# Kernel optimization log

Measured on AMD Instinct MI355X. Metric: run time of the kernel, lower is better.

Reference implementation:

```python
import jax, jax.numpy as jnp
import numpy as np
import math

B, T, C, H = 4, 1024, 1024, 16
D = C // H
EPS = 1e-5


def layer_norm(x, w, b):
    mu = jnp.mean(x, axis=-1, keepdims=True)
    var = jnp.mean(jnp.square(x - mu), axis=-1, keepdims=True)
    return (x - mu) * jax.lax.rsqrt(var + EPS) * w + b


def setup_inputs() -> dict:
    key = jax.random.key(0)
    ks = jax.random.split(key, 8)
    s = 0.02
    return {
        "x": jax.random.normal(ks[0], (B, T, C), jnp.float32),
        "attention_mask": jnp.ones((B, T), jnp.float32),
        "ln1_w": jnp.ones((C,), jnp.float32),
        "ln1_b": jnp.zeros((C,), jnp.float32),
        "w_attn": jax.random.normal(ks[1], (C, 3 * C), jnp.float32) * s,
        "b_attn": jnp.zeros((3 * C,), jnp.float32),
        "w_proj": jax.random.normal(ks[2], (C, C), jnp.float32) * s,
        "b_proj": jnp.zeros((C,), jnp.float32),
        "threshold": jnp.float32(0.0005),  # (layer_idx+1)/n_layer * final_token_threshold
        "ln2_w": jnp.ones((C,), jnp.float32),
        "ln2_b": jnp.zeros((C,), jnp.float32),
        "w_fc": jax.random.normal(ks[3], (C, 4 * C), jnp.float32) * s,
        "b_fc": jnp.zeros((4 * C,), jnp.float32),
        "w_fc2": jax.random.normal(ks[4], (4 * C, C), jnp.float32) * s,
        "b_fc2": jnp.zeros((C,), jnp.float32),
    }


def reference(x, attention_mask, ln1_w, ln1_b, w_attn, b_attn, w_proj, b_proj,
              threshold, ln2_w, ln2_b, w_fc, b_fc, w_fc2, b_fc2):
    # ---- attention (eval mode, dropout=0; hard masking_mode) ----
    h = layer_norm(x, ln1_w, ln1_b)
    qkv = h @ w_attn + b_attn                      # (B,T,3C)
    q, k, v = jnp.split(qkv, 3, axis=-1)
    q = q.reshape(B, T, H, D).transpose(0, 2, 1, 3)  # (B,H,T,D)
    k = k.reshape(B, T, H, D).transpose(0, 2, 1, 3)
    v = v.reshape(B, T, H, D).transpose(0, 2, 1, 3)

    scale = 1.0 / math.sqrt(D)
    logits = jnp.einsum("bhqd,bhkd->bhqk", q, k) * scale  # (B,H,T,T)
    causal = jnp.tril(jnp.ones((T, T), bool))
    neg_inf = jnp.float32(-jnp.inf)
    logits = jnp.where(causal[None, None], logits, neg_inf)
    # key-side validity mask (applied in original's manual pass; mask is all-ones
    # here so flash-path y == softmax(causal logits) @ v as well)
    logits = jnp.where(attention_mask[:, None, None, :] == 0, neg_inf, logits)
    att = jax.nn.softmax(logits, axis=-1)

    y = jnp.einsum("bhqk,bhkd->bhqd", att, v)      # (B,H,T,D)
    importance = att.mean(axis=1).mean(axis=1)     # (B,T): mean over heads, then queries

    y = y.transpose(0, 2, 1, 3).reshape(B, T, C)
    x = x + (y @ w_proj + b_proj)

    # ---- hard pruning mask ----
    pruning_mask = (importance >= threshold).astype(x.dtype)
    combined_mask = attention_mask * pruning_mask
    x = x * combined_mask[:, :, None]

    # ---- MLP ----
    h2 = layer_norm(x, ln2_w, ln2_b)
    f = jax.nn.gelu(h2 @ w_fc + b_fc, approximate=False)
    x = x + (f @ w_fc2 + b_fc2)

    pruning_loss = jnp.float32(0.0)  # hard mode -> always 0
    return (x, combined_mask, pruning_loss)
```

## Files before the change

### kernel.cpp

```cpp
#include <hip/hip_runtime.h>
#include <cstdint>
#include <cstring>

typedef unsigned short u16;
typedef short bf16x8 __attribute__((ext_vector_type(8)));
typedef float f32x4 __attribute__((ext_vector_type(4)));

#define MFMA16(a,b,c) __builtin_amdgcn_mfma_f32_16x16x32_bf16(a,b,c,0,0,0)


__device__ __forceinline__ u16 f2bf(float f) {
  union { float f; uint32_t u; } un; un.f = f;
  uint32_t u = un.u;
  u += 0x7FFFu + ((u >> 16) & 1u);
  return (u16)(u >> 16);
}

__device__ __forceinline__ void gl_lds16(const void* g, void* l) {
  __builtin_amdgcn_global_load_lds(
      (__attribute__((address_space(1))) void*)(const_cast<void*>(g)),
      (__attribute__((address_space(3))) void*)l, 16, 0, 0);
}


__global__ __launch_bounds__(256) void transpose_to_bf16(
    const float* __restrict__ W, u16* __restrict__ Wt, int K, int N)
{
  __shared__ float tile[32][33];
  int kt = blockIdx.y * 32, nt = blockIdx.x * 32;
  int tx = threadIdx.x, ty = threadIdx.y;
#pragma unroll
  for (int i = 0; i < 4; ++i)
    tile[ty + i * 8][tx] = W[(size_t)(kt + ty + i * 8) * N + nt + tx];
  __syncthreads();
#pragma unroll
  for (int i = 0; i < 4; ++i)
    Wt[(size_t)(nt + ty + i * 8) * K + kt + tx] = f2bf(tile[tx][ty + i * 8]);
}


__global__ __launch_bounds__(256) void ln_bf16(
    const float* __restrict__ x, const float* __restrict__ wt,
    const float* __restrict__ bs, u16* __restrict__ out)
{
  int row = blockIdx.x;
  int tid = threadIdx.x, lane = tid & 63, w = tid >> 6;
  const float* xr = x + (size_t)row * 1024;
  float4 v = *(const float4*)(xr + tid * 4);
  float s = v.x + v.y + v.z + v.w;
  float sq = v.x * v.x + v.y * v.y + v.z * v.z + v.w * v.w;
#pragma unroll
  for (int o = 1; o < 64; o <<= 1) { s += __shfl_xor(s, o); sq += __shfl_xor(sq, o); }
  __shared__ float ls[4], lq[4];
  if (lane == 0) { ls[w] = s; lq[w] = sq; }
  __syncthreads();
  s = ls[0] + ls[1] + ls[2] + ls[3];
  sq = lq[0] + lq[1] + lq[2] + lq[3];
  float mu = s * (1.f / 1024.f);
  float var = sq * (1.f / 1024.f) - mu * mu;
  float rstd = rsqrtf(var + 1e-5f);
  float4 wv = *(const float4*)(wt + tid * 4);
  float4 bv = *(const float4*)(bs + tid * 4);
  ushort4 o4;
  o4.x = f2bf((v.x - mu) * rstd * wv.x + bv.x);
  o4.y = f2bf((v.y - mu) * rstd * wv.y + bv.y);
  o4.z = f2bf((v.z - mu) * rstd * wv.z + bv.z);
  o4.w = f2bf((v.w - mu) * rstd * wv.w + bv.w);
  *(ushort4*)(out + (size_t)row * 1024 + tid * 4) = o4;
}


__device__ __forceinline__ void gemm_mainloop_db(
    const u16* __restrict__ Abase, const u16* __restrict__ Bbase,
    int lda, int ldb, int nIter, f32x4 acc[4][4])
{
  __shared__ __align__(16) u16 lA[2][128 * 32];
  __shared__ __align__(16) u16 lB[2][128 * 32];

  const int tid = threadIdx.x;
  const int lane = tid & 63;
  const int w = tid >> 6;
  const int wr = (w >> 1) * 64;
  const int wc = (w & 1) * 64;
  const int laneM = lane & 15;
  const int laneK = (lane >> 4) * 8;

#pragma unroll
  for (int i = 0; i < 4; ++i)
#pragma unroll
    for (int j = 0; j < 4; ++j)
      acc[i][j] = f32x4{0.f, 0.f, 0.f, 0.f};

  const int off0 = w * 1024 + lane * 16;
  const int off1 = off0 + 4096;
  const int rA0 = off0 >> 6, cb0 = off0 & 63;
  const int rA1 = off1 >> 6, cb1 = off1 & 63;

  const size_t sA = (size_t)lda * 2;
  const size_t sB = (size_t)ldb * 2;
  const char* pA0 = (const char*)Abase + (size_t)rA0 * sA + cb0;
  const char* pA1 = (const char*)Abase + (size_t)rA1 * sA + cb1;
  const char* pB0 = (const char*)Bbase + (size_t)rA0 * sB + cb0;
  const char* pB1 = (const char*)Bbase + (size_t)rA1 * sB + cb1;
  char* dA0 = (char*)&lA[0][0] + off0;
  char* dA1 = (char*)&lA[0][0] + off1;
  char* dB0 = (char*)&lB[0][0] + off0;
  char* dB1 = (char*)&lB[0][0] + off1;

  gl_lds16(pA0, dA0); gl_lds16(pA1, dA1);
  gl_lds16(pB0, dB0); gl_lds16(pB1, dB1);
  pA0 += 64; pA1 += 64; pB0 += 64; pB1 += 64;
  __syncthreads();

  for (int it = 0; it < nIter; ++it) {
    const int cur = it & 1;
    const int nb = cur ^ 1;
    if (it + 1 < nIter) {
      gl_lds16(pA0, dA0 + nb * 8192);
      gl_lds16(pA1, dA1 + nb * 8192);
      gl_lds16(pB0, dB0 + nb * 8192);
      gl_lds16(pB1, dB1 + nb * 8192);
      pA0 += 64; pA1 += 64; pB0 += 64; pB1 += 64;
    }
    const u16* aRd = &lA[cur][(wr + laneM) * 32 + laneK];
    const u16* bRd = &lB[cur][(wc + laneM) * 32 + laneK];
    bf16x8 af[4], bfr[4];
#pragma unroll
    for (int t = 0; t < 4; ++t) {
      af[t]  = *(const bf16x8*)(aRd + t * 16 * 32);
      bfr[t] = *(const bf16x8*)(bRd + t * 16 * 32);
    }
#pragma unroll
    for (int i = 0; i < 4; ++i)
#pragma unroll
      for (int j = 0; j < 4; ++j)
        acc[i][j] = MFMA16(af[i], bfr[j], acc[i][j]);
    if (it + 1 < nIter) __syncthreads();
  }
}


__global__ __launch_bounds__(256) void gemm_qkv(
    const u16* __restrict__ A, const u16* __restrict__ Bt,
    const float* __restrict__ bias,
    u16* __restrict__ qo, u16* __restrict__ ko, u16* __restrict__ vo)
{
  f32x4 acc[4][4];
  int m0 = blockIdx.y * 128, n0 = blockIdx.x * 128;
  gemm_mainloop_db(A + (size_t)m0 * 1024, Bt + (size_t)n0 * 1024, 1024, 1024, 32, acc);
  const int lane = threadIdx.x & 63, w = threadIdx.x >> 6;
  const int wr = (w >> 1) * 64, wc = (w & 1) * 64;
  const int laneM = lane & 15, q4 = lane >> 4;
  const int which = (n0 >> 10);
#pragma unroll
  for (int ti = 0; ti < 4; ++ti) {
#pragma unroll
    for (int tj = 0; tj < 4; ++tj) {
      int n = n0 + wc + tj * 16 + laneM;
      int c = n & 1023;
      int hh = c >> 6, d = c & 63;
      float bval = bias[n];
      if (which == 2) {
        int m0r = m0 + wr + ti * 16 + q4 * 4;
        int b = m0r >> 10, t0 = m0r & 1023;
        ushort4 o4;
        o4.x = f2bf(acc[ti][tj][0] + bval);
        o4.y = f2bf(acc[ti][tj][1] + bval);
        o4.z = f2bf(acc[ti][tj][2] + bval);
        o4.w = f2bf(acc[ti][tj][3] + bval);
        *(ushort4*)&vo[((size_t)((b * 16 + hh) * 64 + d)) * 1024 + t0] = o4;
      } else {
        u16* dst = (which == 0) ? qo : ko;
#pragma unroll
        for (int r = 0; r < 4; ++r) {
          int m = m0 + wr + ti * 16 + q4 * 4 + r;
          int b = m >> 10, t = m & 1023;
          dst[((size_t)((b * 16 + hh) * 1024 + t)) * 64 + d] = f2bf(acc[ti][tj][r] + bval);
        }
      }
    }
  }
}

__global__ __launch_bounds__(256) void gemm_proj(
    const u16* __restrict__ A, const u16* __restrict__ Bt,
    const float* __restrict__ bias, const float* __restrict__ xin,
    const float* __restrict__ maskv, float* __restrict__ x2)
{
  f32x4 acc[4][4];
  int m0 = blockIdx.y * 128, n0 = blockIdx.x * 128;
  gemm_mainloop_db(A + (size_t)m0 * 1024, Bt + (size_t)n0 * 1024, 1024, 1024, 32, acc);
  const int lane = threadIdx.x & 63, w = threadIdx.x >> 6;
  const int wr = (w >> 1) * 64, wc = (w & 1) * 64;
  const int laneM = lane & 15, q4 = lane >> 4;
#pragma unroll
  for (int ti = 0; ti < 4; ++ti) {
#pragma unroll
    for (int tj = 0; tj < 4; ++tj) {
      int n = n0 + wc + tj * 16 + laneM;
      float bval = bias[n];
#pragma unroll
      for (int r = 0; r < 4; ++r) {
        int m = m0 + wr + ti * 16 + q4 * 4 + r;
        float v = xin[(size_t)m * 1024 + n] + acc[ti][tj][r] + bval;
        x2[(size_t)m * 1024 + n] = v * maskv[m];
      }
    }
  }
}

__global__ __launch_bounds__(256) void gemm_fc(
    const u16* __restrict__ A, const u16* __restrict__ Bt,
    const float* __restrict__ bias, u16* __restrict__ fo)
{
  f32x4 acc[4][4];
  int m0 = blockIdx.y * 128, n0 = blockIdx.x * 128;
  gemm_mainloop_db(A + (size_t)m0 * 1024, Bt + (size_t)n0 * 1024, 1024, 1024, 32, acc);
  const int lane = threadIdx.x & 63, w = threadIdx.x >> 6;
  const int wr = (w >> 1) * 64, wc = (w & 1) * 64;
  const int laneM = lane & 15, q4 = lane >> 4;
#pragma unroll
  for (int ti = 0; ti < 4; ++ti) {
#pragma unroll
    for (int tj = 0; tj < 4; ++tj) {
      int n = n0 + wc + tj * 16 + laneM;
      float bval = bias[n];
#pragma unroll
      for (int r = 0; r < 4; ++r) {
        int m = m0 + wr + ti * 16 + q4 * 4 + r;
        float v = acc[ti][tj][r] + bval;
        float g = 0.5f * v * (1.f + erff(v * 0.70710678118654752f));
        fo[(size_t)m * 4096 + n] = f2bf(g);
      }
    }
  }
}

__global__ __launch_bounds__(256) void prefill_out(
    const float* __restrict__ x2, const float* __restrict__ bias,
    float* __restrict__ out)
{
  int i = blockIdx.x * 256 + threadIdx.x;
  int col4 = i & 255;
  float4 v = ((const float4*)x2)[i];
  float4 b = ((const float4*)bias)[col4];
  float4 o; o.x = v.x + b.x; o.y = v.y + b.y; o.z = v.z + b.z; o.w = v.w + b.w;
  ((float4*)out)[i] = o;
}

__global__ __launch_bounds__(256) void gemm_fc2_splitk(
    const u16* __restrict__ A, const u16* __restrict__ Bt,
    float* __restrict__ out)
{
  f32x4 acc[4][4];
  int m0 = blockIdx.y * 128, n0 = blockIdx.x * 128, k0 = blockIdx.z * 1024;
  gemm_mainloop_db(A + (size_t)m0 * 4096 + k0, Bt + (size_t)n0 * 4096 + k0,
                   4096, 4096, 32, acc);
  const int lane = threadIdx.x & 63, w = threadIdx.x >> 6;
  const int wr = (w >> 1) * 64, wc = (w & 1) * 64;
  const int laneM = lane & 15, q4 = lane >> 4;
#pragma unroll
  for (int ti = 0; ti < 4; ++ti) {
#pragma unroll
    for (int tj = 0; tj < 4; ++tj) {
      int n = n0 + wc + tj * 16 + laneM;
#pragma unroll
      for (int r = 0; r < 4; ++r) {
        int m = m0 + wr + ti * 16 + q4 * 4 + r;
        atomicAdd(&out[(size_t)m * 1024 + n], acc[ti][tj][r]);
      }
    }
  }
}


__global__ __launch_bounds__(256) void attn_fwd(
    const u16* __restrict__ qb, const u16* __restrict__ kb, const u16* __restrict__ vtb,
    u16* __restrict__ yb, float* __restrict__ part)
{
  const int bh = blockIdx.x;
  const int qbi = 15 - blockIdx.y;
  const int b = bh >> 4, h = bh & 15;
  const int tid = threadIdx.x, lane = tid & 63, w = tid >> 6;
  const int q0 = qbi * 64;
  const int laneM = lane & 15, q4 = lane >> 4;
  const float scale = 0.125f;

  __shared__ __align__(16) u16 lK[64 * 72];
  __shared__ __align__(16) u16 lV[64 * 72];
  __shared__ __align__(16) u16 lP[4][16 * 72];

  const u16* qrow = qb + ((size_t)(bh * 1024 + q0 + w * 16 + laneM)) * 64 + q4 * 8;
  bf16x8 qf0 = *(const bf16x8*)qrow;
  bf16x8 qf1 = *(const bf16x8*)(qrow + 32);

  const int nkt = qbi + 1;
  const int srow = tid >> 3;
  const int scol = (tid & 7) * 8;
  const u16* kbase = kb + (size_t)bh * 65536;
  const u16* vbase = vtb + (size_t)bh * 65536;

  float lrow[4] = {0.f, 0.f, 0.f, 0.f};
  for (int kt = 0; kt < nkt; ++kt) {
#pragma unroll
    for (int p = 0; p < 2; ++p) {
      int row = srow + p * 32;
      *(uint4*)&lK[row * 72 + scol] =
          *(const uint4*)(kbase + (size_t)(kt * 64 + row) * 64 + scol);
    }
    __syncthreads();
#pragma unroll
    for (int tj = 0; tj < 4; ++tj) {
      const u16* kp = &lK[(tj * 16 + laneM) * 72 + q4 * 8];
      bf16x8 k0 = *(const bf16x8*)kp;
      bf16x8 k1 = *(const bf16x8*)(kp + 32);
      f32x4 z = {0.f, 0.f, 0.f, 0.f};
      z = MFMA16(qf0, k0, z);
      z = MFMA16(qf1, k1, z);
      int kc = kt * 64 + tj * 16 + laneM;
#pragma unroll
      for (int r = 0; r < 4; ++r) {
        int qg = q0 + w * 16 + q4 * 4 + r;
        lrow[r] += (kc <= qg) ? __expf(z[r] * scale) : 0.f;
      }
    }
    __syncthreads();
  }
  float linv[4];
#pragma unroll
  for (int r = 0; r < 4; ++r) {
    float s = lrow[r];
    s += __shfl_xor(s, 1); s += __shfl_xor(s, 2);
    s += __shfl_xor(s, 4); s += __shfl_xor(s, 8);
    linv[r] = 1.f / s;
  }

  f32x4 o_[4];
#pragma unroll
  for (int dt = 0; dt < 4; ++dt) o_[dt] = f32x4{0.f, 0.f, 0.f, 0.f};

  for (int kt = 0; kt < nkt; ++kt) {
#pragma unroll
    for (int p = 0; p < 2; ++p) {
      int row = srow + p * 32;
      *(uint4*)&lK[row * 72 + scol] =
          *(const uint4*)(kbase + (size_t)(kt * 64 + row) * 64 + scol);
      *(uint4*)&lV[row * 72 + scol] =
          *(const uint4*)(vbase + (size_t)row * 1024 + kt * 64 + scol);
    }
    __syncthreads();
    u16* lPw = &lP[w][0];
#pragma unroll
    for (int tj = 0; tj < 4; ++tj) {
      const u16* kp = &lK[(tj * 16 + laneM) * 72 + q4 * 8];
      bf16x8 k0 = *(const bf16x8*)kp;
      bf16x8 k1 = *(const bf16x8*)(kp + 32);
      f32x4 z = {0.f, 0.f, 0.f, 0.f};
      z = MFMA16(qf0, k0, z);
      z = MFMA16(qf1, k1, z);
      int kc = kt * 64 + tj * 16 + laneM;
      float cs = 0.f;
#pragma unroll
      for (int r = 0; r < 4; ++r) {
        int qg = q0 + w * 16 + q4 * 4 + r;
        float pv = (kc <= qg) ? __expf(z[r] * scale) * linv[r] : 0.f;
        cs += pv;
        lPw[(q4 * 4 + r) * 72 + tj * 16 + laneM] = f2bf(pv);
      }
      cs += __shfl_xor(cs, 16);
      cs += __shfl_xor(cs, 32);
      if (lane < 16)
        atomicAdd(&part[(size_t)bh * 1024 + kt * 64 + tj * 16 + lane], cs);
    }
#pragma unroll
    for (int ss = 0; ss < 2; ++ss) {
      bf16x8 pf = *(const bf16x8*)&lP[w][laneM * 72 + ss * 32 + q4 * 8];
#pragma unroll
      for (int dt = 0; dt < 4; ++dt) {
        bf16x8 vf = *(const bf16x8*)&lV[(dt * 16 + laneM) * 72 + ss * 32 + q4 * 8];
        o_[dt] = MFMA16(pf, vf, o_[dt]);
      }
    }
    __syncthreads();
  }

#pragma unroll
  for (int dt = 0; dt < 4; ++dt)
#pragma unroll
    for (int r = 0; r < 4; ++r) {
      int qg = q0 + w * 16 + q4 * 4 + r;
      yb[((size_t)(b * 1024 + qg)) * 1024 + h * 64 + dt * 16 + laneM] = f2bf(o_[dt][r]);
    }
}


__global__ __launch_bounds__(256) void finalize_mask(
    const float* __restrict__ part, const float* __restrict__ amask,
    const float* __restrict__ thr, float* __restrict__ mask_ws,
    float* __restrict__ out_mask, float* __restrict__ out_loss)
{
  int i = blockIdx.x * 256 + threadIdx.x;
  if (i >= 4096) return;
  int b = i >> 10;
  int t = i & 1023;
  float s = 0.f;
#pragma unroll
  for (int hh = 0; hh < 16; ++hh) s += part[(size_t)(b * 16 + hh) * 1024 + t];
  float imp = s * (1.0f / 16384.0f);
  float mv = (imp >= thr[0]) ? amask[i] : 0.f;
  mask_ws[i] = mv;
  out_mask[i] = mv;
  if (i == 0) out_loss[0] = 0.f;
}


extern "C" void kernel_launch(void* const* d_in, const int* in_sizes, int n_in,
                              void* d_out, int out_size, void* d_ws, size_t ws_size,
                              hipStream_t stream) {
  const float* x      = (const float*)d_in[0];
  const float* amask  = (const float*)d_in[1];
  const float* ln1w   = (const float*)d_in[2];
  const float* ln1b   = (const float*)d_in[3];
  const float* w_attn = (const float*)d_in[4];
  const float* b_attn = (const float*)d_in[5];
  const float* w_proj = (const float*)d_in[6];
  const float* b_proj = (const float*)d_in[7];
  const float* thr    = (const float*)d_in[8];
  const float* ln2w   = (const float*)d_in[9];
  const float* ln2b   = (const float*)d_in[10];
  const float* w_fc   = (const float*)d_in[11];
  const float* b_fc   = (const float*)d_in[12];
  const float* w_fc2  = (const float*)d_in[13];
  const float* b_fc2  = (const float*)d_in[14];
  float* out = (float*)d_out;

  char* ws = (char*)d_ws;
  size_t off = 0;
  auto alloc = [&](size_t bytes) -> char* {
    char* p = ws + off;
    off += (bytes + 255) & ~(size_t)255;
    return p;
  };
  u16* wattnT = (u16*)alloc((size_t)3072 * 1024 * 2);
  u16* wprojT = (u16*)alloc((size_t)1024 * 1024 * 2);
  u16* wfcT   = (u16*)alloc((size_t)4096 * 1024 * 2);
  u16* wfc2T  = (u16*)alloc((size_t)1024 * 4096 * 2);
  u16* hbuf   = (u16*)alloc((size_t)4096 * 1024 * 2);
  u16* qbuf   = (u16*)alloc((size_t)64 * 1024 * 64 * 2);
  u16* kbuf   = (u16*)alloc((size_t)64 * 1024 * 64 * 2);
  u16* vtbuf  = (u16*)alloc((size_t)64 * 64 * 1024 * 2);
  u16* ybuf   = (u16*)alloc((size_t)4096 * 1024 * 2);
  float* part = (float*)alloc((size_t)64 * 1024 * 4);
  float* maskws = (float*)alloc((size_t)4096 * 4);
  float* x2   = (float*)alloc((size_t)4096 * 1024 * 4);
  u16* h2     = (u16*)alloc((size_t)4096 * 1024 * 2);
  u16* fbuf   = (u16*)alloc((size_t)4096 * 4096 * 2);

  dim3 tb(32, 8);
  transpose_to_bf16<<<dim3(96, 32),  tb, 0, stream>>>(w_attn, wattnT, 1024, 3072);
  transpose_to_bf16<<<dim3(32, 32),  tb, 0, stream>>>(w_proj, wprojT, 1024, 1024);
  transpose_to_bf16<<<dim3(128, 32), tb, 0, stream>>>(w_fc,   wfcT,   1024, 4096);
  transpose_to_bf16<<<dim3(32, 128), tb, 0, stream>>>(w_fc2,  wfc2T,  4096, 1024);

  hipMemsetAsync(part, 0, (size_t)64 * 1024 * 4, stream);

  ln_bf16<<<4096, 256, 0, stream>>>(x, ln1w, ln1b, hbuf);

  gemm_qkv<<<dim3(24, 32), 256, 0, stream>>>(hbuf, wattnT, b_attn, qbuf, kbuf, vtbuf);

  attn_fwd<<<dim3(64, 16), 256, 0, stream>>>(qbuf, kbuf, vtbuf, ybuf, part);

  finalize_mask<<<16, 256, 0, stream>>>(part, amask, thr, maskws,
                                        out + 4194304, out + 4198400);

  gemm_proj<<<dim3(8, 32), 256, 0, stream>>>(ybuf, wprojT, b_proj, x, maskws, x2);

  ln_bf16<<<4096, 256, 0, stream>>>(x2, ln2w, ln2b, h2);

  gemm_fc<<<dim3(32, 32), 256, 0, stream>>>(h2, wfcT, b_fc, fbuf);

  prefill_out<<<4096, 256, 0, stream>>>(x2, b_fc2, out);

  gemm_fc2_splitk<<<dim3(8, 32, 4), 256, 0, stream>>>(fbuf, wfc2T, out);
}
```

Before: 419.1 us.

## Merge weight transposes, enlarge attention query tile, replace fc2 atomics with partial buffers

The four weight-transpose launches are merged into one kernel that picks its matrix from the block index. Attention now uses 128-query tiles with two 16-row sub-tiles per wave, so each K/V tile loaded into LDS is reused twice as much and the grid is halved. The fc2 split-K drops from four to two slices. Each slice writes plain stores into a partial buffer that reuses the dead q/vt scratch memory, and a finalize kernel sums both partials with the residual and bias, removing the float atomics. The cost is fewer attention blocks, which gives less parallelism and coarser causal load balance, plus an extra pass that reads two fp32 partials.

```diff
diff --git a/kernel.cpp b/kernel.cpp
--- a/kernel.cpp
+++ b/kernel.cpp
@@ -23,11 +23,20 @@
 }
 
 
-__global__ __launch_bounds__(256) void transpose_to_bf16(
-    const float* __restrict__ W, u16* __restrict__ Wt, int K, int N)
+__global__ __launch_bounds__(256) void transpose_all(
+    const float* __restrict__ wa, const float* __restrict__ wp,
+    const float* __restrict__ wf, const float* __restrict__ wf2,
+    u16* __restrict__ wat, u16* __restrict__ wpt,
+    u16* __restrict__ wft, u16* __restrict__ wf2t)
 {
   __shared__ float tile[32][33];
-  int kt = blockIdx.y * 32, nt = blockIdx.x * 32;
+  int id = blockIdx.x;
+  const float* W; u16* Wt; int K, N, bx, by;
+  if (id < 3072)      { W = wa;  Wt = wat;  K = 1024; N = 3072; bx = id % 96;  by = id / 96; }
+  else if (id < 4096) { id -= 3072; W = wp;  Wt = wpt;  K = 1024; N = 1024; bx = id % 32; by = id / 32; }
+  else if (id < 8192) { id -= 4096; W = wf;  Wt = wft;  K = 1024; N = 4096; bx = id % 128; by = id / 128; }
+  else                { id -= 8192; W = wf2; Wt = wf2t; K = 4096; N = 1024; bx = id % 32; by = id / 32; }
+  int kt = by * 32, nt = bx * 32;
   int tx = threadIdx.x, ty = threadIdx.y;
 #pragma unroll
   for (int i = 0; i < 4; ++i)
@@ -236,26 +245,15 @@
   }
 }
 
-__global__ __launch_bounds__(256) void prefill_out(
-    const float* __restrict__ x2, const float* __restrict__ bias,
-    float* __restrict__ out)
-{
-  int i = blockIdx.x * 256 + threadIdx.x;
-  int col4 = i & 255;
-  float4 v = ((const float4*)x2)[i];
-  float4 b = ((const float4*)bias)[col4];
-  float4 o; o.x = v.x + b.x; o.y = v.y + b.y; o.z = v.z + b.z; o.w = v.w + b.w;
-  ((float4*)out)[i] = o;
-}
-
 __global__ __launch_bounds__(256) void gemm_fc2_splitk(
     const u16* __restrict__ A, const u16* __restrict__ Bt,
-    float* __restrict__ out)
+    float* __restrict__ p0, float* __restrict__ p1)
 {
   f32x4 acc[4][4];
-  int m0 = blockIdx.y * 128, n0 = blockIdx.x * 128, k0 = blockIdx.z * 1024;
-  gemm_mainloop_db(A + (size_t)m0 * 4096 + k0, Bt + (size_t)n0 * 4096 + k0,
-                   4096, 4096, 32, acc);
+  int m0 = blockIdx.y * 128, n0 = blockIdx.x * 128, kz = blockIdx.z;
+  gemm_mainloop_db(A + (size_t)m0 * 4096 + kz * 2048,
+                   Bt + (size_t)n0 * 4096 + kz * 2048, 4096, 4096, 64, acc);
+  float* p = kz ? p1 : p0;
   const int lane = threadIdx.x & 63, w = threadIdx.x >> 6;
   const int wr = (w >> 1) * 64, wc = (w & 1) * 64;
   const int laneM = lane & 15, q4 = lane >> 4;
@@ -267,10 +265,29 @@
 #pragma unroll
       for (int r = 0; r < 4; ++r) {
         int m = m0 + wr + ti * 16 + q4 * 4 + r;
-        atomicAdd(&out[(size_t)m * 1024 + n], acc[ti][tj][r]);
-      }
-    }
-  }
+        p[(size_t)m * 1024 + n] = acc[ti][tj][r];
+      }
+    }
+  }
+}
+
+__global__ __launch_bounds__(256) void fc2_finalize(
+    const float* __restrict__ x2, const float* __restrict__ bias,
+    const float* __restrict__ p0, const float* __restrict__ p1,
+    float* __restrict__ out)
+{
+  int i = blockIdx.x * 256 + threadIdx.x;
+  int col4 = i & 255;
+  float4 a = ((const float4*)x2)[i];
+  float4 b = ((const float4*)bias)[col4];
+  float4 u = ((const float4*)p0)[i];
+  float4 v = ((const float4*)p1)[i];
+  float4 o;
+  o.x = a.x + b.x + u.x + v.x;
+  o.y = a.y + b.y + u.y + v.y;
+  o.z = a.z + b.z + u.z + v.z;
+  o.w = a.w + b.w + u.w + v.w;
+  ((float4*)out)[i] = o;
 }
 
 
@@ -279,28 +296,32 @@
     u16* __restrict__ yb, float* __restrict__ part)
 {
   const int bh = blockIdx.x;
-  const int qbi = 15 - blockIdx.y;
+  const int qbi = 7 - blockIdx.y;
   const int b = bh >> 4, h = bh & 15;
   const int tid = threadIdx.x, lane = tid & 63, w = tid >> 6;
-  const int q0 = qbi * 64;
+  const int q0 = qbi * 128;
   const int laneM = lane & 15, q4 = lane >> 4;
   const float scale = 0.125f;
 
   __shared__ __align__(16) u16 lK[64 * 72];
   __shared__ __align__(16) u16 lV[64 * 72];
-  __shared__ __align__(16) u16 lP[4][16 * 72];
-
-  const u16* qrow = qb + ((size_t)(bh * 1024 + q0 + w * 16 + laneM)) * 64 + q4 * 8;
-  bf16x8 qf0 = *(const bf16x8*)qrow;
-  bf16x8 qf1 = *(const bf16x8*)(qrow + 32);
-
-  const int nkt = qbi + 1;
+  __shared__ __align__(16) u16 lP[4][32 * 72];
+
+  bf16x8 qf[2][2];
+#pragma unroll
+  for (int qs = 0; qs < 2; ++qs) {
+    const u16* qrow = qb + ((size_t)(bh * 1024 + q0 + w * 32 + qs * 16 + laneM)) * 64 + q4 * 8;
+    qf[qs][0] = *(const bf16x8*)qrow;
+    qf[qs][1] = *(const bf16x8*)(qrow + 32);
+  }
+
+  const int nkt = 2 * qbi + 2;
   const int srow = tid >> 3;
   const int scol = (tid & 7) * 8;
   const u16* kbase = kb + (size_t)bh * 65536;
   const u16* vbase = vtb + (size_t)bh * 65536;
 
-  float lrow[4] = {0.f, 0.f, 0.f, 0.f};
+  float lrow[2][4] = {{0.f,0.f,0.f,0.f},{0.f,0.f,0.f,0.f}};
   for (int kt = 0; kt < nkt; ++kt) {
 #pragma unroll
     for (int p = 0; p < 2; ++p) {
@@ -314,30 +335,37 @@
       const u16* kp = &lK[(tj * 16 + laneM) * 72 + q4 * 8];
       bf16x8 k0 = *(const bf16x8*)kp;
       bf16x8 k1 = *(const bf16x8*)(kp + 32);
-      f32x4 z = {0.f, 0.f, 0.f, 0.f};
-      z = MFMA16(qf0, k0, z);
-      z = MFMA16(qf1, k1, z);
       int kc = kt * 64 + tj * 16 + laneM;
 #pragma unroll
-      for (int r = 0; r < 4; ++r) {
-        int qg = q0 + w * 16 + q4 * 4 + r;
-        lrow[r] += (kc <= qg) ? __expf(z[r] * scale) : 0.f;
+      for (int qs = 0; qs < 2; ++qs) {
+        f32x4 z = {0.f, 0.f, 0.f, 0.f};
+        z = MFMA16(qf[qs][0], k0, z);
+        z = MFMA16(qf[qs][1], k1, z);
+#pragma unroll
+        for (int r = 0; r < 4; ++r) {
+          int qg = q0 + w * 32 + qs * 16 + q4 * 4 + r;
+          lrow[qs][r] += (kc <= qg) ? __expf(z[r] * scale) : 0.f;
+        }
       }
     }
     __syncthreads();
   }
-  float linv[4];
-#pragma unroll
-  for (int r = 0; r < 4; ++r) {
-    float s = lrow[r];
-    s += __shfl_xor(s, 1); s += __shfl_xor(s, 2);
-    s += __shfl_xor(s, 4); s += __shfl_xor(s, 8);
-    linv[r] = 1.f / s;
-  }
-
-  f32x4 o_[4];
-#pragma unroll
-  for (int dt = 0; dt < 4; ++dt) o_[dt] = f32x4{0.f, 0.f, 0.f, 0.f};
+  float linv[2][4];
+#pragma unroll
+  for (int qs = 0; qs < 2; ++qs)
+#pragma unroll
+    for (int r = 0; r < 4; ++r) {
+      float s = lrow[qs][r];
+      s += __shfl_xor(s, 1); s += __shfl_xor(s, 2);
+      s += __shfl_xor(s, 4); s += __shfl_xor(s, 8);
+      linv[qs][r] = 1.f / s;
+    }
+
+  f32x4 o_[2][4];
+#pragma unroll
+  for (int qs = 0; qs < 2; ++qs)
+#pragma unroll
+    for (int dt = 0; dt < 4; ++dt) o_[qs][dt] = f32x4{0.f, 0.f, 0.f, 0.f};
 
   for (int kt = 0; kt < nkt; ++kt) {
 #pragma unroll
@@ -355,17 +383,20 @@
       const u16* kp = &lK[(tj * 16 + laneM) * 72 + q4 * 8];
       bf16x8 k0 = *(const bf16x8*)kp;
       bf16x8 k1 = *(const bf16x8*)(kp + 32);
-      f32x4 z = {0.f, 0.f, 0.f, 0.f};
-      z = MFMA16(qf0, k0, z);
-      z = MFMA16(qf1, k1, z);
       int kc = kt * 64 + tj * 16 + laneM;
       float cs = 0.f;
 #pragma unroll
-      for (int r = 0; r < 4; ++r) {
-        int qg = q0 + w * 16 + q4 * 4 + r;
-        float pv = (kc <= qg) ? __expf(z[r] * scale) * linv[r] : 0.f;
-        cs += pv;
-        lPw[(q4 * 4 + r) * 72 + tj * 16 + laneM] = f2bf(pv);
+      for (int qs = 0; qs < 2; ++qs) {
+        f32x4 z = {0.f, 0.f, 0.f, 0.f};
+        z = MFMA16(qf[qs][0], k0, z);
+        z = MFMA16(qf[qs][1], k1, z);
+#pragma unroll
+        for (int r = 0; r < 4; ++r) {
+          int qg = q0 + w * 32 + qs * 16 + q4 * 4 + r;
+          float pv = (kc <= qg) ? __expf(z[r] * scale) * linv[qs][r] : 0.f;
+          cs += pv;
+          lPw[(qs * 16 + q4 * 4 + r) * 72 + tj * 16 + laneM] = f2bf(pv);
+        }
       }
       cs += __shfl_xor(cs, 16);
       cs += __shfl_xor(cs, 32);
@@ -374,23 +405,28 @@
     }
 #pragma unroll
     for (int ss = 0; ss < 2; ++ss) {
-      bf16x8 pf = *(const bf16x8*)&lP[w][laneM * 72 + ss * 32 + q4 * 8];
-#pragma unroll
-      for (int dt = 0; dt < 4; ++dt) {
-        bf16x8 vf = *(const bf16x8*)&lV[(dt * 16 + laneM) * 72 + ss * 32 + q4 * 8];
-        o_[dt] = MFMA16(pf, vf, o_[dt]);
+#pragma unroll
+      for (int qs = 0; qs < 2; ++qs) {
+        bf16x8 pf = *(const bf16x8*)&lP[w][(qs * 16 + laneM) * 72 + ss * 32 + q4 * 8];
+#pragma unroll
+        for (int dt = 0; dt < 4; ++dt) {
+          bf16x8 vf = *(const bf16x8*)&lV[(dt * 16 + laneM) * 72 + ss * 32 + q4 * 8];
+          o_[qs][dt] = MFMA16(pf, vf, o_[qs][dt]);
+        }
       }
     }
     __syncthreads();
   }
 
 #pragma unroll
-  for (int dt = 0; dt < 4; ++dt)
-#pragma unroll
-    for (int r = 0; r < 4; ++r) {
-      int qg = q0 + w * 16 + q4 * 4 + r;
-      yb[((size_t)(b * 1024 + qg)) * 1024 + h * 64 + dt * 16 + laneM] = f2bf(o_[dt][r]);
-    }
+  for (int qs = 0; qs < 2; ++qs)
+#pragma unroll
+    for (int dt = 0; dt < 4; ++dt)
+#pragma unroll
+      for (int r = 0; r < 4; ++r) {
+        int qg = q0 + w * 32 + qs * 16 + q4 * 4 + r;
+        yb[((size_t)(b * 1024 + qg)) * 1024 + h * 64 + dt * 16 + laneM] = f2bf(o_[qs][dt][r]);
+      }
 }
 
 
@@ -456,11 +492,11 @@
   u16* h2     = (u16*)alloc((size_t)4096 * 1024 * 2);
   u16* fbuf   = (u16*)alloc((size_t)4096 * 4096 * 2);
 
-  dim3 tb(32, 8);
-  transpose_to_bf16<<<dim3(96, 32),  tb, 0, stream>>>(w_attn, wattnT, 1024, 3072);
-  transpose_to_bf16<<<dim3(32, 32),  tb, 0, stream>>>(w_proj, wprojT, 1024, 1024);
-  transpose_to_bf16<<<dim3(128, 32), tb, 0, stream>>>(w_fc,   wfcT,   1024, 4096);
-  transpose_to_bf16<<<dim3(32, 128), tb, 0, stream>>>(w_fc2,  wfc2T,  4096, 1024);
+  float* p0 = (float*)qbuf;
+  float* p1 = (float*)vtbuf;
+
+  transpose_all<<<12288, dim3(32, 8), 0, stream>>>(
+      w_attn, w_proj, w_fc, w_fc2, wattnT, wprojT, wfcT, wfc2T);
 
   hipMemsetAsync(part, 0, (size_t)64 * 1024 * 4, stream);
 
@@ -468,7 +504,7 @@
 
   gemm_qkv<<<dim3(24, 32), 256, 0, stream>>>(hbuf, wattnT, b_attn, qbuf, kbuf, vtbuf);
 
-  attn_fwd<<<dim3(64, 16), 256, 0, stream>>>(qbuf, kbuf, vtbuf, ybuf, part);
+  attn_fwd<<<dim3(64, 8), 256, 0, stream>>>(qbuf, kbuf, vtbuf, ybuf, part);
 
   finalize_mask<<<16, 256, 0, stream>>>(part, amask, thr, maskws,
                                         out + 4194304, out + 4198400);
@@ -479,7 +515,7 @@
 
   gemm_fc<<<dim3(32, 32), 256, 0, stream>>>(h2, wfcT, b_fc, fbuf);
 
-  prefill_out<<<4096, 256, 0, stream>>>(x2, b_fc2, out);
-
-  gemm_fc2_splitk<<<dim3(8, 32, 4), 256, 0, stream>>>(fbuf, wfc2T, out);
-}
+  gemm_fc2_splitk<<<dim3(8, 32, 2), 256, 0, stream>>>(fbuf, wfc2T, p0, p1);
+
+  fc2_finalize<<<4096, 256, 0, stream>>>(x2, b_fc2, p0, p1, out);
+}
```

Measured after the change: 413.0 us. About the same (-1.5%).
